# Performance work log

Hardware: AMD Instinct MI355X
Metric: run time of the kernel (lower is better)

The kernel has to match this reference:

```python
import jax, jax.numpy as jnp
import numpy as np

DIM = 1024
HEADS = 16
B, N = 4, 1024

def setup_inputs() -> dict:
    key = jax.random.key(0)
    k1, k2, k3 = jax.random.split(key, 3)
    x = jax.random.normal(k1, (B, N, DIM), dtype=jnp.float32)
    # xavier-uniform-ish init scale
    Wqkv = jax.random.normal(k2, (3 * DIM, DIM), dtype=jnp.float32) * (1.0 / np.sqrt(DIM))
    bqkv = jnp.zeros((3 * DIM,), dtype=jnp.float32)
    W1 = jax.random.normal(k3, (DIM, DIM), dtype=jnp.float32) * (1.0 / np.sqrt(DIM))
    b1 = jnp.zeros((DIM,), dtype=jnp.float32)
    return {"x": x, "Wqkv": Wqkv, "bqkv": bqkv, "W1": W1, "b1": b1}

def reference(x, Wqkv, bqkv, W1, b1):
    b, n, dim = x.shape
    h = HEADS
    d = dim // h
    scale = dim ** (-0.5)  # NOTE: module scales by full dim, not head dim
    qkv = x @ Wqkv.T + bqkv  # [b, n, 3*dim]
    qkv = qkv.reshape(b, n, 3, h, d)
    q = jnp.transpose(qkv[:, :, 0], (0, 2, 1, 3))  # [b, h, n, d]
    k = jnp.transpose(qkv[:, :, 1], (0, 2, 1, 3))
    v = jnp.transpose(qkv[:, :, 2], (0, 2, 1, 3))
    dots = jnp.einsum('bhid,bhjd->bhij', q, k) * scale
    attn = jax.nn.softmax(dots, axis=-1)
    out = jnp.einsum('bhij,bhjd->bhid', attn, v)
    out = jnp.transpose(out, (0, 2, 1, 3)).reshape(b, n, dim)
    out = out @ W1.T + b1
    return out
```

## Files before the change

kernel.cpp:

```cpp
#include <hip/hip_runtime.h>
#include <cmath>

typedef __bf16 bf16;
typedef __bf16 bf16x8 __attribute__((ext_vector_type(8)));
typedef __bf16 bf16x4 __attribute__((ext_vector_type(4)));
typedef float f32x4 __attribute__((ext_vector_type(4)));

#define MFMA16(a, b, c) __builtin_amdgcn_mfma_f32_16x16x32_bf16(a, b, c, 0, 0, 0)

__device__ __forceinline__ void load_lds16(const void* g, void* l) {
    __builtin_amdgcn_global_load_lds(
        (const __attribute__((address_space(1))) void*)g,
        (__attribute__((address_space(3))) void*)l, 16, 0, 0);
}

__device__ __forceinline__ bf16x8 load8(const bf16* p) { return *(const bf16x8*)p; }
__device__ __forceinline__ bf16x8 load8(const float* p) {
    float4 f0 = *(const float4*)p;
    float4 f1 = *(const float4*)(p + 4);
    bf16x8 r;
    r[0] = (bf16)f0.x; r[1] = (bf16)f0.y; r[2] = (bf16)f0.z; r[3] = (bf16)f0.w;
    r[4] = (bf16)f1.x; r[5] = (bf16)f1.y; r[6] = (bf16)f1.z; r[7] = (bf16)f1.w;
    return r;
}

__global__ __launch_bounds__(256) void cvt3(
    const float* __restrict__ s0, bf16* __restrict__ d0, int n0,
    const float* __restrict__ s1, bf16* __restrict__ d1, int n1,
    const float* __restrict__ s2, bf16* __restrict__ d2, int n2)
{
    int i = blockIdx.x * 256 + threadIdx.x;
    const float* s; bf16* d; int base;
    if (i < n0)                { s = s0; d = d0; base = i; }
    else if (i < n0 + n1)      { s = s1; d = d1; base = i - n0; }
    else if (i < n0 + n1 + n2) { s = s2; d = d2; base = i - n0 - n1; }
    else return;
    *(bf16x8*)(d + (size_t)base * 8) = load8(s + (size_t)base * 8);
}

template <int EPI, typename TB, int BN>
__global__ __launch_bounds__(256) void gemm_bt(
    const bf16* __restrict__ A, const TB* __restrict__ Bm,
    const float* __restrict__ bias,
    bf16* __restrict__ qo, bf16* __restrict__ ko, bf16* __restrict__ vto,
    float* __restrict__ C, int M, int N, int K)
{
    constexpr int WN = BN / 2;
    constexpr int JN = WN / 16;
    constexpr int SLOTS = (128 + BN) * 8;

    __shared__ bf16 As[128 * 64];
    __shared__ bf16 Bs[BN * 64];

    const int tid = threadIdx.x;
    const int l   = tid & 63;
    const int w   = tid >> 6;
    const int wm  = w & 1, wn = w >> 1;
    const int l15 = l & 15;
    const int g   = l >> 4;
    const int swz = l15 & 7;
    const int m0  = blockIdx.y * 128;
    const int n0  = blockIdx.x * BN;

    f32x4 acc[4][JN] = {};

    for (int k0 = 0; k0 < K; k0 += 64) {
        __syncthreads();
        #pragma unroll
        for (int it = 0; it < SLOTS / 256; ++it) {
            int s = it * 256 + w * 64 + l;
            if (s < 1024) {
                int row = s >> 3, pc = s & 7;
                int lc  = pc ^ (row & 7);
                load_lds16(A + (size_t)(m0 + row) * K + k0 + lc * 8, &As[s * 8]);
            } else {
                int t = s - 1024;
                int row = t >> 3, pc = t & 7;
                int lc  = pc ^ (row & 7);
                if constexpr (sizeof(TB) == 2) {
                    load_lds16(Bm + (size_t)(n0 + row) * K + k0 + lc * 8, &Bs[t * 8]);
                } else {
                    *(bf16x8*)&Bs[t * 8] = load8(Bm + (size_t)(n0 + row) * K + k0 + lc * 8);
                }
            }
        }
        __syncthreads();
        #pragma unroll
        for (int kk = 0; kk < 64; kk += 32) {
            bf16x8 aF[4], bF[JN];
            #pragma unroll
            for (int i = 0; i < 4; ++i)
                aF[i] = *(const bf16x8*)&As[(wm * 64 + i * 16 + l15) * 64
                                            + ((((kk >> 3) + g) ^ swz) * 8)];
            #pragma unroll
            for (int j = 0; j < JN; ++j)
                bF[j] = *(const bf16x8*)&Bs[(wn * WN + j * 16 + l15) * 64
                                            + ((((kk >> 3) + g) ^ swz) * 8)];
            #pragma unroll
            for (int i = 0; i < 4; ++i)
                #pragma unroll
                for (int j = 0; j < JN; ++j)
                    acc[i][j] = MFMA16(aF[i], bF[j], acc[i][j]);
        }
    }

    #pragma unroll
    for (int j = 0; j < JN; ++j) {
        int gcol = n0 + wn * WN + j * 16 + l15;
        float bv = bias[gcol];
        if (EPI == 0) {
            int which = gcol >> 10;
            int h  = (gcol >> 6) & 15;
            int dd = gcol & 63;
            if (which == 2) {
                #pragma unroll
                for (int i = 0; i < 4; ++i) {
                    int grow0 = m0 + wm * 64 + i * 16 + g * 4;
                    int b     = grow0 >> 10;
                    int npos  = grow0 & 1023;
                    size_t bh = (size_t)(b * 16 + h);
                    bf16x4 pv;
                    #pragma unroll
                    for (int r = 0; r < 4; ++r)
                        pv[r] = (bf16)(acc[i][j][r] + bv);
                    *(bf16x4*)&vto[(bh * 64 + dd) * 1024 + npos] = pv;
                }
            } else {
                #pragma unroll
                for (int i = 0; i < 4; ++i) {
                    #pragma unroll
                    for (int r = 0; r < 4; ++r) {
                        int grow = m0 + wm * 64 + i * 16 + g * 4 + r;
                        int b    = grow >> 10;
                        int npos = grow & 1023;
                        float v  = acc[i][j][r] + bv;
                        size_t bh = (size_t)(b * 16 + h);
                        if (which == 0)
                            qo[(bh * 1024 + npos) * 64 + dd] = (bf16)v;
                        else
                            ko[(bh * 1024 + npos) * 64 + dd] = (bf16)v;
                    }
                }
            }
        } else {
            #pragma unroll
            for (int i = 0; i < 4; ++i)
                #pragma unroll
                for (int r = 0; r < 4; ++r) {
                    int grow = m0 + wm * 64 + i * 16 + g * 4 + r;
                    C[(size_t)grow * N + gcol] = acc[i][j][r] + bv;
                }
        }
    }
}

__global__ __launch_bounds__(512, 8) void attn_fused(
    const bf16* __restrict__ qb, const bf16* __restrict__ kb,
    const bf16* __restrict__ vtb, bf16* __restrict__ attn)
{
    __shared__ bf16 Ks[2][64 * 64];
    __shared__ bf16 Vts[2][64 * 64];
    __shared__ bf16 Ps[8][16][32];

    const int tid = threadIdx.x;
    const int l   = tid & 63;
    const int w   = tid >> 6;
    const int wq  = w & 3;
    const int wh  = w >> 2;
    const int l15 = l & 15;
    const int g   = l >> 4;
    const int swz = l15 & 7;
    const int bid = blockIdx.x;
    const int bh  = bid & 63;
    const int qc  = bid >> 6;
    const int m0  = qc * 64;

    const bf16* q_bh  = qb  + (size_t)bh * 65536;
    const bf16* k_bh  = kb  + (size_t)bh * 65536;
    const bf16* vt_bh = vtb + (size_t)bh * 65536;

    bf16x8 qf[2];
    #pragma unroll
    for (int kk = 0; kk < 2; ++kk)
        qf[kk] = *(const bf16x8*)(q_bh + (size_t)(m0 + wq * 16 + l15) * 64
                                  + kk * 32 + g * 8);

    f32x4 o[4] = {};
    float lsum = 0.f;

    const float C_EXP = 0.04508422f;

    auto stage = [&](int buf, int j0) {
        int s   = tid;
        int row = s >> 3, pc = s & 7;
        int lc  = pc ^ (row & 7);
        load_lds16(k_bh + (size_t)(j0 + row) * 64 + lc * 8, &Ks[buf][s * 8]);
        load_lds16(vt_bh + (size_t)row * 1024 + j0 + lc * 8, &Vts[buf][s * 8]);
    };

    stage(0, 0);

    for (int t = 0; t < 16; ++t) {
        const int c = t & 1;
        __syncthreads();
        if (t < 15) stage(c ^ 1, (t + 1) * 64);

        f32x4 s4[2] = {};
        #pragma unroll
        for (int kk = 0; kk < 2; ++kk) {
            bf16x8 kf[2];
            #pragma unroll
            for (int jsl = 0; jsl < 2; ++jsl)
                kf[jsl] = *(const bf16x8*)&Ks[c][((wh * 2 + jsl) * 16 + l15) * 64
                                                 + (((kk * 4 + g) ^ swz) * 8)];
            __builtin_amdgcn_s_setprio(1);
            #pragma unroll
            for (int jsl = 0; jsl < 2; ++jsl)
                s4[jsl] = MFMA16(kf[jsl], qf[kk], s4[jsl]);
            __builtin_amdgcn_s_setprio(0);
        }

        #pragma unroll
        for (int jsl = 0; jsl < 2; ++jsl) {
            bf16x4 pk;
            float ps = 0.f;
            #pragma unroll
            for (int r = 0; r < 4; ++r) {
                float p = exp2f(s4[jsl][r] * C_EXP);
                ps += p;
                pk[r] = (bf16)p;
            }
            lsum += ps;
            *(bf16x4*)&Ps[w][l15][(((jsl * 2 + (g >> 1)) ^ (l15 & 3)) * 8)
                                  + (g & 1) * 4] = pk;
        }

        bf16x8 vf[4];
        #pragma unroll
        for (int ns = 0; ns < 4; ++ns)
            vf[ns] = *(const bf16x8*)&Vts[c][(ns * 16 + l15) * 64
                                             + (((wh * 4 + g) ^ swz) * 8)];
        bf16x8 pf = *(const bf16x8*)&Ps[w][l15][(g ^ (l15 & 3)) * 8];
        __builtin_amdgcn_s_setprio(1);
        #pragma unroll
        for (int ns = 0; ns < 4; ++ns)
            o[ns] = MFMA16(pf, vf[ns], o[ns]);
        __builtin_amdgcn_s_setprio(0);
    }

    float tden = lsum;
    tden += __shfl_xor(tden, 16);
    tden += __shfl_xor(tden, 32);

    float* R  = (float*)&Ks[0][0];
    float* DN = (float*)&Vts[0][0];
    __syncthreads();
    if (wh == 1) {
        #pragma unroll
        for (int ns = 0; ns < 4; ++ns)
            *(f32x4*)&R[((wq * 64 + l) * 4 + ns) * 4] = o[ns];
        DN[wq * 64 + l] = tden;
    }
    __syncthreads();
    if (wh == 0) {
        #pragma unroll
        for (int ns = 0; ns < 4; ++ns)
            o[ns] += *(const f32x4*)&R[((wq * 64 + l) * 4 + ns) * 4];
        tden += DN[wq * 64 + l];

        #pragma unroll
        for (int r = 0; r < 4; ++r) {
            float inv = 1.0f / __shfl(tden, g * 4 + r);
            int grow = m0 + wq * 16 + g * 4 + r;
            size_t obase = ((size_t)(bh >> 4) * 1024 + grow) * 1024 + (bh & 15) * 64;
            #pragma unroll
            for (int ns = 0; ns < 4; ++ns)
                attn[obase + ns * 16 + l15] = (bf16)(o[ns][r] * inv);
        }
    }
}

extern "C" void kernel_launch(void* const* d_in, const int* in_sizes, int n_in,
                              void* d_out, int out_size, void* d_ws, size_t ws_size,
                              hipStream_t stream)
{
    const float* x    = (const float*)d_in[0];
    const float* Wqkv = (const float*)d_in[1];
    const float* bqkv = (const float*)d_in[2];
    const float* W1   = (const float*)d_in[3];
    const float* b1   = (const float*)d_in[4];
    float* out = (float*)d_out;

    const size_t SEG = (size_t)4 * 16 * 1024 * 64;
    bf16* xbf  = (bf16*)d_ws;
    bf16* qb   = xbf + SEG;
    bf16* kb   = qb + SEG;
    bf16* vtb  = kb + SEG;
    bf16* attnb = xbf;
    bf16* wqkvbf = vtb + SEG;
    bf16* w1bf   = wqkvbf + 3145728;

    const bool cw = ws_size >= (size_t)(5 * SEG) * sizeof(bf16);

    const int nx = 524288;
    const int nw = cw ? 393216 : 0;
    const int n1 = cw ? 131072 : 0;
    const int tot = nx + nw + n1;
    cvt3<<<dim3((tot + 255) / 256), 256, 0, stream>>>(
        x, xbf, nx, Wqkv, wqkvbf, nw, W1, w1bf, n1);

    if (cw)
        gemm_bt<0, bf16, 128><<<dim3(24, 32), 256, 0, stream>>>(
            xbf, wqkvbf, bqkv, qb, kb, vtb, nullptr, 4096, 3072, 1024);
    else
        gemm_bt<0, float, 128><<<dim3(24, 32), 256, 0, stream>>>(
            xbf, Wqkv, bqkv, qb, kb, vtb, nullptr, 4096, 3072, 1024);

    attn_fused<<<dim3(1024), 512, 0, stream>>>(qb, kb, vtb, attnb);

    if (cw)
        gemm_bt<1, bf16, 64><<<dim3(16, 32), 256, 0, stream>>>(
            attnb, w1bf, b1, nullptr, nullptr, nullptr, out, 4096, 1024, 1024);
    else
        gemm_bt<1, float, 64><<<dim3(16, 32), 256, 0, stream>>>(
            attnb, W1, b1, nullptr, nullptr, nullptr, out, 4096, 1024, 1024);
}
```

Before: 164.9 us.

## Add 256x256-tile double-buffered 8-wave QKV GEMM kernel

```diff
diff --git a/kernel.cpp b/kernel.cpp
--- a/kernel.cpp
+++ b/kernel.cpp
@@ -36,6 +36,126 @@
     else if (i < n0 + n1 + n2) { s = s2; d = d2; base = i - n0 - n1; }
     else return;
     *(bf16x8*)(d + (size_t)base * 8) = load8(s + (size_t)base * 8);
+}
+
+__global__ __launch_bounds__(512, 2) void gemm_qkv8(
+    const bf16* __restrict__ A, const bf16* __restrict__ Bm,
+    const float* __restrict__ bias,
+    bf16* __restrict__ qo, bf16* __restrict__ ko, bf16* __restrict__ vto,
+    int M, int N, int K)
+{
+    __shared__ bf16 As[2][256 * 64];
+    __shared__ bf16 Bs[2][256 * 64];
+
+    const int tid = threadIdx.x;
+    const int l   = tid & 63;
+    const int w   = tid >> 6;
+    const int wm  = w >> 2;
+    const int wn  = w & 3;
+    const int l15 = l & 15;
+    const int g   = l >> 4;
+    const int swz = l15 & 7;
+    const int m0  = blockIdx.y * 256;
+    const int n0  = blockIdx.x * 256;
+
+    f32x4 acc[8][4] = {};
+
+    auto stage = [&](int buf, int k0) {
+        #pragma unroll
+        for (int it = 0; it < 4; ++it) {
+            int s   = it * 512 + tid;
+            int row = s >> 3, pc = s & 7;
+            int lc  = pc ^ (row & 7);
+            load_lds16(A + (size_t)(m0 + row) * K + k0 + lc * 8, &As[buf][s * 8]);
+        }
+        #pragma unroll
+        for (int it = 0; it < 4; ++it) {
+            int s   = it * 512 + tid;
+            int row = s >> 3, pc = s & 7;
+            int lc  = pc ^ (row & 7);
+            load_lds16(Bm + (size_t)(n0 + row) * K + k0 + lc * 8, &Bs[buf][s * 8]);
+        }
+    };
+
+    stage(0, 0);
+
+    for (int kt = 0; kt < 16; ++kt) {
+        const int c = kt & 1;
+        asm volatile("s_waitcnt vmcnt(0)" ::: "memory");
+        __builtin_amdgcn_s_barrier();
+        if (kt < 15) stage(c ^ 1, (kt + 1) << 6);
+
+        bf16x8 bF[4][2];
+        #pragma unroll
+        for (int nj = 0; nj < 4; ++nj)
+            #pragma unroll
+            for (int kk = 0; kk < 2; ++kk)
+                bF[nj][kk] = *(const bf16x8*)&Bs[c][(wn * 64 + nj * 16 + l15) * 64
+                                                    + (((kk * 4 + g) ^ swz) * 8)];
+        #pragma unroll
+        for (int q = 0; q < 4; ++q) {
+            bf16x8 aF[2][2];
+            #pragma unroll
+            for (int mi2 = 0; mi2 < 2; ++mi2)
+                #pragma unroll
+                for (int kk = 0; kk < 2; ++kk)
+                    aF[mi2][kk] = *(const bf16x8*)&As[c][(wm * 128 + (q * 2 + mi2) * 16 + l15) * 64
+                                                         + (((kk * 4 + g) ^ swz) * 8)];
+            __builtin_amdgcn_s_barrier();
+            asm volatile("s_waitcnt lgkmcnt(0)" ::: "memory");
+            __builtin_amdgcn_sched_barrier(0);
+            __builtin_amdgcn_s_setprio(1);
+            #pragma unroll
+            for (int kk = 0; kk < 2; ++kk)
+                #pragma unroll
+                for (int mi2 = 0; mi2 < 2; ++mi2)
+                    #pragma unroll
+                    for (int nj = 0; nj < 4; ++nj)
+                        acc[q * 2 + mi2][nj] = MFMA16(aF[mi2][kk], bF[nj][kk],
+                                                      acc[q * 2 + mi2][nj]);
+            __builtin_amdgcn_s_setprio(0);
+            __builtin_amdgcn_s_barrier();
+        }
+    }
+
+    #pragma unroll
+    for (int nj = 0; nj < 4; ++nj) {
+        int gcol = n0 + wn * 64 + nj * 16 + l15;
+        float bv = bias[gcol];
+        int which = gcol >> 10;
+        int h  = (gcol >> 6) & 15;
+        int dd = gcol & 63;
+        if (which == 2) {
+            #pragma unroll
+            for (int mi = 0; mi < 8; ++mi) {
+                int grow0 = m0 + wm * 128 + mi * 16 + g * 4;
+                int b     = grow0 >> 10;
+                int npos  = grow0 & 1023;
+                size_t bh = (size_t)(b * 16 + h);
+                bf16x4 pv;
+                #pragma unroll
+                for (int r = 0; r < 4; ++r)
+                    pv[r] = (bf16)(acc[mi][nj][r] + bv);
+                *(bf16x4*)&vto[(bh * 64 + dd) * 1024 + npos] = pv;
+            }
+        } else {
+            #pragma unroll
+            for (int mi = 0; mi < 8; ++mi) {
+                #pragma unroll
+                for (int r = 0; r < 4; ++r) {
+                    int grow = m0 + wm * 128 + mi * 16 + g * 4 + r;
+                    int b    = grow >> 10;
+                    int npos = grow & 1023;
+                    float v  = acc[mi][nj][r] + bv;
+                    size_t bh = (size_t)(b * 16 + h);
+                    if (which == 0)
+                        qo[(bh * 1024 + npos) * 64 + dd] = (bf16)v;
+                    else
+                        ko[(bh * 1024 + npos) * 64 + dd] = (bf16)v;
+                }
+            }
+        }
+    }
 }
 
 template <int EPI, typename TB, int BN>
@@ -310,8 +430,8 @@
         x, xbf, nx, Wqkv, wqkvbf, nw, W1, w1bf, n1);
 
     if (cw)
-        gemm_bt<0, bf16, 128><<<dim3(24, 32), 256, 0, stream>>>(
-            xbf, wqkvbf, bqkv, qb, kb, vtb, nullptr, 4096, 3072, 1024);
+        gemm_qkv8<<<dim3(12, 16), 512, 0, stream>>>(
+            xbf, wqkvbf, bqkv, qb, kb, vtb, 4096, 3072, 1024);
     else
         gemm_bt<0, float, 128><<<dim3(24, 32), 256, 0, stream>>>(
             xbf, Wqkv, bqkv, qb, kb, vtb, nullptr, 4096, 3072, 1024);
```

After: 184.0 us. 11.6% more time.
